# Optimization experiments

Measured on AMD Instinct MI355X. Metric: run time of the kernel, lower is better.

The kernel has to match this reference:

```python
import jax, jax.numpy as jnp
import numpy as np

EPS = 1e-5  # torch GroupNorm default


def setup_inputs() -> dict:
    key = jax.random.key(0)
    ks = jax.random.split(key, 6)
    C = 256
    B, F, H, W = 1, 8, 32, 32
    scale = 1.0 / np.sqrt(C)  # keep logits well-scaled
    return {
        "x": jax.random.normal(ks[0], (B, C, F, H, W), dtype=jnp.float32),
        "gn_w": jnp.ones((C,), jnp.float32),
        "gn_b": jnp.zeros((C,), jnp.float32),
        "qw": jax.random.normal(ks[1], (C, C), jnp.float32) * scale,
        "qb": jnp.zeros((C,), jnp.float32),
        "kw": jax.random.normal(ks[2], (C, C), jnp.float32) * scale,
        "kb": jnp.zeros((C,), jnp.float32),
        "vw": jax.random.normal(ks[3], (C, C), jnp.float32) * scale,
        "vb": jnp.zeros((C,), jnp.float32),
        "ow": jax.random.normal(ks[4], (C, C), jnp.float32) * scale,
        "ob": jnp.zeros((C,), jnp.float32),
    }


def reference(x, gn_w, gn_b, qw, qb, kw, kb, vw, vb, ow, ob):
    B, C, F, H, W = x.shape
    N = F * H * W
    # GroupNorm(1, C): normalize over (C,F,H,W) per sample, per-channel affine
    mean = jnp.mean(x, axis=(1, 2, 3, 4), keepdims=True)
    var = jnp.var(x, axis=(1, 2, 3, 4), keepdims=True)
    xn = (x - mean) * jax.lax.rsqrt(var + EPS)
    xn = xn * gn_w[None, :, None, None, None] + gn_b[None, :, None, None, None]
    xf = xn.reshape(B, C, N)  # [B, C, N]
    # 1x1x1 Conv3d == channel matmul
    q = jnp.einsum('oc,bcn->bon', qw, xf) + qb[None, :, None]
    k = jnp.einsum('oc,bcn->bon', kw, xf) + kb[None, :, None]
    v = jnp.einsum('oc,bcn->bon', vw, xf) + vb[None, :, None]
    # scores[b, n_q, n_k] = q^T k, scaled by C^-0.5
    scores = jnp.einsum('bcn,bcm->bnm', q, k) * (C ** -0.5)
    weights = jax.nn.softmax(scores, axis=-1)  # over keys
    # attention[b, c, n_q] = sum_m v[b,c,m] * weights[b,n_q,m]
    att = jnp.einsum('bcm,bnm->bcn', v, weights)
    att = jnp.einsum('oc,bcn->bon', ow, att) + ob[None, :, None]
    return xn + att.reshape(B, C, F, H, W)
```

## Files before the change

### kernel.cpp

```cpp
#include <hip/hip_runtime.h>
#include <hip/hip_bf16.h>
#include <cstdint>

#define NSP 8192
#define CCH 256
#define KBLK 32
#define NSPLIT 8
#define KEYS_PER_SPLIT 1024
#define NTILES 32

typedef __attribute__((ext_vector_type(4))) float f32x4;
typedef __attribute__((ext_vector_type(16))) float f32x16;
typedef __attribute__((ext_vector_type(8))) short bf16x8;
typedef __attribute__((ext_vector_type(2))) unsigned int u32x2;

__device__ __forceinline__ ushort f2bf(float f) {
  union { float f; uint32_t u; } v; v.f = f;
  uint32_t r = (v.u + 0x7FFFu + ((v.u >> 16) & 1u)) >> 16;
  return (ushort)r;
}
__device__ __forceinline__ float bf2f(ushort u) {
  union { uint32_t u; float f; } v; v.u = ((uint32_t)u) << 16; return v.f;
}
__device__ __forceinline__ uint32_t pk2bf(float lo, float hi) {
  __hip_bfloat162 h = __float22bfloat162_rn({lo, hi});
  union { __hip_bfloat162 h; uint32_t u; } c; c.h = h; return c.u;
}

__device__ __forceinline__ void gload_lds16(const void* g, void* l) {
  auto gp = (const __attribute__((address_space(1))) uint32_t*)(uintptr_t)g;
  auto lp = (__attribute__((address_space(3))) uint32_t*)(uint32_t)(uintptr_t)l;
  __builtin_amdgcn_global_load_lds(gp, lp, 16, 0, 0);
}

__device__ __forceinline__ void perm32swap(uint32_t& a, uint32_t& b) {
#if __has_builtin(__builtin_amdgcn_permlane32_swap)
  u32x2 r = __builtin_amdgcn_permlane32_swap(a, b, false, false);
  a = r[0]; b = r[1];
#else
  uint32_t sa = __shfl_xor((int)a, 32), sb = __shfl_xor((int)b, 32);
  bool lo = (threadIdx.x & 63) < 32;
  uint32_t na = lo ? a : sb;
  uint32_t nb = lo ? sa : b;
  a = na; b = nb;
#endif
}

__global__ __launch_bounds__(256) void k_stats1(const float* __restrict__ x,
                                                float* __restrict__ part) {
  int t = threadIdx.x, b = blockIdx.x;
  float s = 0.f, ss = 0.f;
  const float4* x4 = (const float4*)x;
  for (int i = 0; i < 4; ++i) {
    float4 v = x4[(size_t)i * 131072 + b * 256 + t];
    s += v.x + v.y + v.z + v.w;
    ss += v.x * v.x + v.y * v.y + v.z * v.z + v.w * v.w;
  }
  for (int m = 1; m < 64; m <<= 1) { s += __shfl_xor(s, m); ss += __shfl_xor(ss, m); }
  __shared__ float ls[4], lss[4];
  int w = t >> 6, lane = t & 63;
  if (lane == 0) { ls[w] = s; lss[w] = ss; }
  __syncthreads();
  if (t == 0) {
    part[b * 2 + 0] = ls[0] + ls[1] + ls[2] + ls[3];
    part[b * 2 + 1] = lss[0] + lss[1] + lss[2] + lss[3];
  }
}

__global__ __launch_bounds__(256) void k_castw(const float* __restrict__ qw, const float* __restrict__ kw,
                                               const float* __restrict__ vw, const float* __restrict__ ow,
                                               ushort* __restrict__ wqkv, ushort* __restrict__ wo,
                                               const float* __restrict__ part, float* __restrict__ stat) {
  if (blockIdx.x == 1024) {
    int t = threadIdx.x;
    float s = 0.f, ss = 0.f;
    for (int i = t; i < 512; i += 256) { s += part[i * 2]; ss += part[i * 2 + 1]; }
    for (int m = 1; m < 64; m <<= 1) { s += __shfl_xor(s, m); ss += __shfl_xor(ss, m); }
    __shared__ float ls[4], lss[4];
    int w = t >> 6, lane = t & 63;
    if (lane == 0) { ls[w] = s; lss[w] = ss; }
    __syncthreads();
    if (t == 0) {
      float sum = ls[0] + ls[1] + ls[2] + ls[3];
      float ssum = lss[0] + lss[1] + lss[2] + lss[3];
      float mean = sum * (1.f / 2097152.f);
      float var = ssum * (1.f / 2097152.f) - mean * mean;
      stat[0] = mean;
      stat[1] = rsqrtf(var + 1e-5f);
    }
    return;
  }
  int idx = blockIdx.x * 256 + threadIdx.x;
  if (idx < 65536) wqkv[idx] = f2bf(qw[idx]);
  else if (idx < 131072) wqkv[idx] = f2bf(kw[idx - 65536]);
  else if (idx < 196608) wqkv[idx] = f2bf(vw[idx - 131072]);
  else wo[idx - 196608] = f2bf(ow[idx - 196608]);
}

__global__ __launch_bounds__(256) void k_norm_t(const float* __restrict__ x,
                                                const float* __restrict__ gw, const float* __restrict__ gb,
                                                const float* __restrict__ stat, ushort* __restrict__ xnT) {
  __shared__ float tile[64][66];
  int n0 = blockIdx.x * 64, c0 = blockIdx.y * 64;
  int t = threadIdx.x, colr = t & 63, rq = t >> 6;
  float mean = stat[0], rinv = stat[1];
  for (int rr = 0; rr < 16; ++rr) {
    int row = rr * 4 + rq;
    int c = c0 + row;
    float v = x[(size_t)c * NSP + n0 + colr];
    tile[row][colr] = (v - mean) * rinv * gw[c] + gb[c];
  }
  __syncthreads();
  for (int rr = 0; rr < 16; ++rr) {
    int rowW = rr * 4 + rq;
    xnT[(size_t)(n0 + rowW) * 256 + c0 + colr] = f2bf(tile[colr][rowW]);
  }
}

__global__ __launch_bounds__(256) void k_qkv(const ushort* __restrict__ xnT, const ushort* __restrict__ wqkv,
                                             const float* __restrict__ qb, const float* __restrict__ kb,
                                             const float* __restrict__ vb,
                                             ushort* __restrict__ qT, ushort* __restrict__ k_tiles,
                                             ushort* __restrict__ v_tiles) {
  __shared__ ushort tile[64][80];
  int nb = blockIdx.x, ob = blockIdx.y;
  int w = threadIdx.x >> 6, lane = threadIdx.x & 63;
  int l16 = lane & 15, kgrp = lane >> 4;
  int n_row = nb * 64 + w * 16 + l16;
  bf16x8 a[8];
  const bf16x8* arow = (const bf16x8*)(xnT + (size_t)n_row * 256);
  for (int ks = 0; ks < 8; ++ks) a[ks] = arow[ks * 4 + kgrp];
  f32x4 acc[4];
  for (int ct = 0; ct < 4; ++ct) {
    int o = ob * 64 + ct * 16 + l16;
    const bf16x8* brow = (const bf16x8*)(wqkv + (size_t)o * 256);
    f32x4 c = {0.f, 0.f, 0.f, 0.f};
    for (int ks = 0; ks < 8; ++ks)
      c = __builtin_amdgcn_mfma_f32_16x16x32_bf16(a[ks], brow[ks * 4 + kgrp], c, 0, 0, 0);
    acc[ct] = c;
  }
  const float SCALE = 0.0625f * 1.44269504088896340736f;
  if (ob < 4) {
    for (int ct = 0; ct < 4; ++ct) {
      int o = ob * 64 + ct * 16 + l16;
      for (int r = 0; r < 4; ++r) {
        int n = nb * 64 + w * 16 + kgrp * 4 + r;
        qT[(size_t)n * 256 + o] = f2bf((acc[ct][r] + qb[o]) * SCALE);
      }
    }
  } else if (ob < 8) {
    for (int ct = 0; ct < 4; ++ct) {
      int o_l = ct * 16 + l16;
      for (int r = 0; r < 4; ++r) {
        int n_l = w * 16 + kgrp * 4 + r;
        tile[n_l][o_l] = f2bf(acc[ct][r] + kb[(ob - 4) * 64 + o_l]);
      }
    }
    __syncthreads();
    for (int j = 0; j < 2; ++j) {
      int idx = j * 256 + threadIdx.x;
      int tile_l = idx >> 8, s = (idx >> 5) & 7, key = idx & 31;
      size_t off = (size_t)(nb * 2 + tile_l) * 16384 +
                   (size_t)((ob - 4) * 8 + s) * 512 + key * 16;
      *(uint4*)((char*)k_tiles + off) = *(const uint4*)&tile[tile_l * 32 + key][s * 8];
    }
  } else {
    for (int ct = 0; ct < 4; ++ct) {
      int o_l = ct * 16 + l16;
      for (int r = 0; r < 4; ++r) {
        int n_l = w * 16 + kgrp * 4 + r;
        tile[o_l][n_l] = f2bf(acc[ct][r] + vb[(ob - 8) * 64 + o_l]);
      }
    }
    __syncthreads();
    for (int j = 0; j < 2; ++j) {
      int idx = j * 256 + threadIdx.x;
      int tile_l = idx >> 8, slot = (idx >> 6) & 3, c_l = idx & 63;
      size_t off = (size_t)(nb * 2 + tile_l) * 8192 + slot * 2048 +
                   (size_t)((ob - 8) * 64 + c_l) * 8;
      *(uint4*)((char*)v_tiles + off * 2) = *(const uint4*)&tile[c_l][tile_l * 32 + slot * 8];
    }
  }
}

__global__ __launch_bounds__(512, 2) void k_attn(const ushort* __restrict__ qT, const ushort* __restrict__ k_tiles,
                                                 const ushort* __restrict__ v_tiles,
                                                 ushort* __restrict__ Opart, float* __restrict__ mpart,
                                                 float* __restrict__ lpart) {
  __shared__ __align__(16) ushort SMEM[32768];
  ushort* k_lds = SMEM;
  ushort* v_lds = SMEM + 16384;

  int bid = blockIdx.x;
  int split = bid & 7, qblk = bid >> 3;
  int t = threadIdx.x, w = t >> 6, lane = t & 63;
  int l31 = lane & 31, lhi = lane >> 5;
  int q0w = qblk * 256 + w * 32;

  bf16x8 qf[16];
  {
    const char* qbase = (const char*)qT + (size_t)(q0w + l31) * 512;
#pragma unroll
    for (int cs = 0; cs < 16; ++cs)
      qf[cs] = *(const bf16x8*)(qbase + cs * 32 + lhi * 16);
  }

  f32x16 acc[8] = {};
  float m_r = -1e30f, l_p = 0.f;
  bf16x8 pf0, pf1;

  const char* kT_b = (const char*)k_tiles + (size_t)split * KEYS_PER_SPLIT * 512;
  const char* v_b = (const char*)v_tiles + (size_t)split * KEYS_PER_SPLIT * 512;

  auto STAGE_K = [&](int tt) {
    const char* ksrc = kT_b + (size_t)tt * 16384 + w * 2048;
    char* kdst = (char*)(k_lds + (tt & 1) * 8192) + w * 2048;
#pragma unroll
    for (int i = 0; i < 2; ++i)
      gload_lds16(ksrc + i * 1024 + lane * 16, kdst + i * 1024);
  };
  auto STAGE_V = [&](int tt) {
    char* vdst = (char*)(v_lds + (tt & 1) * 8192) + w * 2048;
    const char* vsrc = v_b + (size_t)tt * 16384 + w * 2048;
#pragma unroll
    for (int i = 0; i < 2; ++i)
      gload_lds16(vsrc + i * 1024 + lane * 16, vdst + i * 1024);
  };

  auto SOFTMAX_PACK = [&](f32x16& S0) {
    float x0 = fmaxf(S0[0], S0[1]), x1 = fmaxf(S0[2], S0[3]);
    float x2 = fmaxf(S0[4], S0[5]), x3 = fmaxf(S0[6], S0[7]);
    float x4 = fmaxf(S0[8], S0[9]), x5 = fmaxf(S0[10], S0[11]);
    float x6 = fmaxf(S0[12], S0[13]), x7 = fmaxf(S0[14], S0[15]);
    float pm = fmaxf(fmaxf(fmaxf(x0, x1), fmaxf(x2, x3)),
                     fmaxf(fmaxf(x4, x5), fmaxf(x6, x7)));
    pm = fmaxf(pm, __shfl_xor(pm, 32));
    if (!__all(pm <= m_r + 8.f)) {
      float mn = fmaxf(m_r, pm);
      float alpha = __builtin_amdgcn_exp2f(m_r - mn);
      m_r = mn;
      l_p *= alpha;
#pragma unroll
      for (int cb = 0; cb < 8; ++cb)
#pragma unroll
        for (int r = 0; r < 16; ++r) acc[cb][r] *= alpha;
    }
    {
      float t0s = 0.f, t1s = 0.f, t2s = 0.f, t3s = 0.f;
#pragma unroll
      for (int r = 0; r < 16; ++r) {
        S0[r] = __builtin_amdgcn_exp2f(S0[r] - m_r);
        if (r < 4) t0s += S0[r];
        else if (r < 8) t1s += S0[r];
        else if (r < 12) t2s += S0[r];
        else t3s += S0[r];
      }
      l_p += (t0s + t1s) + (t2s + t3s);
    }
    union { uint32_t w[4]; bf16x8 v; } u;
    {
      uint32_t x = pk2bf(S0[0], S0[1]), y = pk2bf(S0[4], S0[5]);
      perm32swap(x, y);
      uint32_t x2_ = pk2bf(S0[2], S0[3]), y2 = pk2bf(S0[6], S0[7]);
      perm32swap(x2_, y2);
      u.w[0] = x; u.w[1] = x2_; u.w[2] = y; u.w[3] = y2;
      pf0 = u.v;
    }
    {
      uint32_t x = pk2bf(S0[8], S0[9]), y = pk2bf(S0[12], S0[13]);
      perm32swap(x, y);
      uint32_t x2_ = pk2bf(S0[10], S0[11]), y2 = pk2bf(S0[14], S0[15]);
      perm32swap(x2_, y2);
      u.w[0] = x; u.w[1] = x2_; u.w[2] = y; u.w[3] = y2;
      pf1 = u.v;
    }
  };

  STAGE_K(0);

  asm volatile("s_waitcnt vmcnt(0) lgkmcnt(0)" ::: "memory");
  __builtin_amdgcn_s_barrier();
  __builtin_amdgcn_sched_barrier(0);
  STAGE_K(1);
  STAGE_V(0);
  {
    const ushort* kl = k_lds;
    f32x16 S0 = {};
    __builtin_amdgcn_s_setprio(1);
#pragma unroll
    for (int cs = 0; cs < 16; ++cs) {
      int slot = cs * 2 + lhi;
      bf16x8 a0 = *(const bf16x8*)(kl + slot * 256 + l31 * 8);
      S0 = __builtin_amdgcn_mfma_f32_32x32x16_bf16(a0, qf[cs], S0, 0, 0, 0);
    }
    __builtin_amdgcn_s_setprio(0);
    SOFTMAX_PACK(S0);
  }

#pragma unroll 1
  for (int tt = 1; tt < NTILES; ++tt) {
    asm volatile("s_waitcnt vmcnt(0) lgkmcnt(0)" ::: "memory");
    __builtin_amdgcn_s_barrier();
    __builtin_amdgcn_sched_barrier(0);
    if (tt + 1 < NTILES) STAGE_K(tt + 1);
    STAGE_V(tt);

    const ushort* kl = k_lds + (tt & 1) * 8192;
    const ushort* vl = v_lds + ((tt - 1) & 1) * 8192;
    f32x16 S0 = {};
    __builtin_amdgcn_s_setprio(1);
#pragma unroll
    for (int cb = 0; cb < 8; ++cb) {
      bf16x8 va0 = *(const bf16x8*)(vl + (0 + lhi) * 2048 + (cb * 32 + l31) * 8);
      acc[cb] = __builtin_amdgcn_mfma_f32_32x32x16_bf16(va0, pf0, acc[cb], 0, 0, 0);
      {
        int slot = 4 * cb + lhi;
        bf16x8 ka = *(const bf16x8*)(kl + slot * 256 + l31 * 8);
        S0 = __builtin_amdgcn_mfma_f32_32x32x16_bf16(ka, qf[2 * cb], S0, 0, 0, 0);
      }
      bf16x8 va1 = *(const bf16x8*)(vl + (2 + lhi) * 2048 + (cb * 32 + l31) * 8);
      acc[cb] = __builtin_amdgcn_mfma_f32_32x32x16_bf16(va1, pf1, acc[cb], 0, 0, 0);
      {
        int slot = 4 * cb + 2 + lhi;
        bf16x8 ka = *(const bf16x8*)(kl + slot * 256 + l31 * 8);
        S0 = __builtin_amdgcn_mfma_f32_32x32x16_bf16(ka, qf[2 * cb + 1], S0, 0, 0, 0);
      }
    }
    __builtin_amdgcn_s_setprio(0);
    SOFTMAX_PACK(S0);
  }

  asm volatile("s_waitcnt vmcnt(0) lgkmcnt(0)" ::: "memory");
  __builtin_amdgcn_s_barrier();
  {
    const ushort* vl = v_lds + ((NTILES - 1) & 1) * 8192;
    __builtin_amdgcn_s_setprio(1);
#pragma unroll
    for (int cb = 0; cb < 8; ++cb) {
      bf16x8 va0 = *(const bf16x8*)(vl + (0 + lhi) * 2048 + (cb * 32 + l31) * 8);
      acc[cb] = __builtin_amdgcn_mfma_f32_32x32x16_bf16(va0, pf0, acc[cb], 0, 0, 0);
      bf16x8 va1 = *(const bf16x8*)(vl + (2 + lhi) * 2048 + (cb * 32 + l31) * 8);
      acc[cb] = __builtin_amdgcn_mfma_f32_32x32x16_bf16(va1, pf1, acc[cb], 0, 0, 0);
    }
    __builtin_amdgcn_s_setprio(0);
  }

  asm volatile("s_waitcnt lgkmcnt(0)" ::: "memory");
  __builtin_amdgcn_s_barrier();

  float l_tot = l_p + __shfl_xor(l_p, 32);

  char* eb = (char*)SMEM + w * 4608;
  size_t gq0 = (size_t)split * NSP + q0w;
#pragma unroll
  for (int ch = 0; ch < 4; ++ch) {
#pragma unroll
    for (int cb2 = 0; cb2 < 2; ++cb2) {
      int cb = ch * 2 + cb2;
#pragma unroll
      for (int g = 0; g < 4; ++g) {
        int cl = cb2 * 32 + g * 8 + 4 * lhi;
        *(uint32_t*)(eb + l31 * 144 + cl * 2) = pk2bf(acc[cb][g * 4 + 0], acc[cb][g * 4 + 1]);
        *(uint32_t*)(eb + l31 * 144 + cl * 2 + 4) = pk2bf(acc[cb][g * 4 + 2], acc[cb][g * 4 + 3]);
      }
    }
    asm volatile("s_waitcnt lgkmcnt(0)" ::: "memory");
    __builtin_amdgcn_sched_barrier(0);
#pragma unroll
    for (int i = 0; i < 4; ++i) {
      int flat = i * 1024 + lane * 16;
      int qr = flat >> 7, off = flat & 127;
      uint4 val = *(const uint4*)(eb + qr * 144 + off);
      *(uint4*)((char*)Opart + (gq0 + qr) * 512 + ch * 128 + off) = val;
    }
    asm volatile("s_waitcnt lgkmcnt(0)" ::: "memory");
    __builtin_amdgcn_sched_barrier(0);
  }
  if (lane < 32) {
    int q = q0w + l31;
    mpart[split * NSP + q] = m_r;
    lpart[split * NSP + q] = l_tot;
  }
}

__global__ __launch_bounds__(256) void k_combine(const ushort* __restrict__ Opart,
                                                 const float* __restrict__ mpart,
                                                 const float* __restrict__ lpart,
                                                 ushort* __restrict__ attT) {
  int q = blockIdx.x * 8 + (threadIdx.x >> 5);
  int c8 = threadIdx.x & 31;
  float M = -1e30f;
#pragma unroll
  for (int s = 0; s < NSPLIT; ++s) M = fmaxf(M, mpart[s * NSP + q]);
  float L = 0.f;
  float av[8] = {};
#pragma unroll
  for (int s = 0; s < NSPLIT; ++s) {
    float ws = __builtin_amdgcn_exp2f(mpart[s * NSP + q] - M);
    L += ws * lpart[s * NSP + q];
    bf16x8 o = *(const bf16x8*)(Opart + ((size_t)s * NSP + q) * 256 + c8 * 8);
#pragma unroll
    for (int j = 0; j < 8; ++j) av[j] += ws * bf2f((ushort)o[j]);
  }
  float rL = 1.f / L;
  uint4 outv;
  outv.x = pk2bf(av[0] * rL, av[1] * rL);
  outv.y = pk2bf(av[2] * rL, av[3] * rL);
  outv.z = pk2bf(av[4] * rL, av[5] * rL);
  outv.w = pk2bf(av[6] * rL, av[7] * rL);
  *(uint4*)(attT + (size_t)q * 256 + c8 * 8) = outv;
}

__global__ __launch_bounds__(256) void k_final(const ushort* __restrict__ attT, const ushort* __restrict__ wo,
                                               const float* __restrict__ ob, const float* __restrict__ x,
                                               const float* __restrict__ gw, const float* __restrict__ gb,
                                               const float* __restrict__ stat, float* __restrict__ out) {
  int nb = blockIdx.x, obk = blockIdx.y;
  int w = threadIdx.x >> 6, lane = threadIdx.x & 63;
  int l16 = lane & 15, kgrp = lane >> 4;
  int orow = obk * 64 + w * 16 + l16;
  bf16x8 a[8];
  const bf16x8* arow = (const bf16x8*)(wo + (size_t)orow * 256);
  for (int ks = 0; ks < 8; ++ks) a[ks] = arow[ks * 4 + kgrp];
  float mean = stat[0], rinv = stat[1];
  f32x4 acc[4];
  for (int ct = 0; ct < 4; ++ct) {
    int n = nb * 64 + ct * 16 + l16;
    const bf16x8* brow = (const bf16x8*)(attT + (size_t)n * 256);
    f32x4 c = {0.f, 0.f, 0.f, 0.f};
    for (int ks = 0; ks < 8; ++ks)
      c = __builtin_amdgcn_mfma_f32_16x16x32_bf16(a[ks], brow[ks * 4 + kgrp], c, 0, 0, 0);
    acc[ct] = c;
  }
  for (int ct = 0; ct < 4; ++ct) {
    for (int r = 0; r < 4; ++r) {
      int o = obk * 64 + w * 16 + kgrp * 4 + r;
      int n = nb * 64 + ct * 16 + l16;
      float xv = x[(size_t)o * NSP + n];
      float xn = (xv - mean) * rinv * gw[o] + gb[o];
      out[(size_t)o * NSP + n] = xn + acc[ct][r] + ob[o];
    }
  }
}

extern "C" void kernel_launch(void* const* d_in, const int* in_sizes, int n_in,
                              void* d_out, int out_size, void* d_ws, size_t ws_size,
                              hipStream_t stream) {
  const float* x = (const float*)d_in[0];
  const float* gw = (const float*)d_in[1];
  const float* gb = (const float*)d_in[2];
  const float* qw = (const float*)d_in[3];
  const float* qbv = (const float*)d_in[4];
  const float* kw = (const float*)d_in[5];
  const float* kbv = (const float*)d_in[6];
  const float* vw = (const float*)d_in[7];
  const float* vbv = (const float*)d_in[8];
  const float* ow = (const float*)d_in[9];
  const float* obv = (const float*)d_in[10];
  float* out = (float*)d_out;
  char* ws = (char*)d_ws;
  const size_t KB = 1024, MB = 1048576;
  float* part = (float*)(ws);
  float* stat = (float*)(ws + 60 * KB);
  ushort* wqkv = (ushort*)(ws + 64 * KB);
  ushort* wo = (ushort*)(ws + 448 * KB);
  float* mpart = (float*)(ws + 64 * KB);
  float* lpart = (float*)(ws + 576 * KB);
  ushort* xnT = (ushort*)(ws + 1 * MB);
  ushort* qT = (ushort*)(ws + 5 * MB);
  ushort* k_tiles = (ushort*)(ws + 9 * MB);
  ushort* v_tiles = (ushort*)(ws + 13 * MB);
  ushort* Opart = (ushort*)(ws + 17 * MB);
  ushort* attT = xnT;

  k_stats1<<<512, 256, 0, stream>>>(x, part);
  k_castw<<<1025, 256, 0, stream>>>(qw, kw, vw, ow, wqkv, wo, part, stat);
  k_norm_t<<<dim3(128, 4), 256, 0, stream>>>(x, gw, gb, stat, xnT);
  k_qkv<<<dim3(128, 12), 256, 0, stream>>>(xnT, wqkv, qbv, kbv, vbv, qT, k_tiles, v_tiles);
  k_attn<<<256, 512, 0, stream>>>(qT, k_tiles, v_tiles, Opart, mpart, lpart);
  k_combine<<<NSP / 8, 256, 0, stream>>>(Opart, mpart, lpart, attT);
  k_final<<<dim3(128, 4), 256, 0, stream>>>(attT, wo, obv, x, gw, gb, stat, out);
}
```

Before: 133.8 us.

## Fuse split combine into output projection and overlap softmax with PV MFMAs

The separate combine kernel, which wrote a bf16 attention buffer, is merged into the final output-projection kernel. It now reduces the split partials into LDS and runs 32x32 MFMAs from there, removing one launch and a global round trip. Inside the attention loop, the QK MFMAs are issued first and the exp2 and max work is interleaved with the second half of the PV MFMAs. The exponentials are computed against the stale running max, and rescaling is deferred until after the tile. The first-tile max now starts from 0 instead of -inf, and correctness relies on the lazy-rescale threshold.

```diff
diff --git a/kernel.cpp b/kernel.cpp
--- a/kernel.cpp
+++ b/kernel.cpp
@@ -206,7 +206,7 @@
   }
 
   f32x16 acc[8] = {};
-  float m_r = -1e30f, l_p = 0.f;
+  float m_r = 0.f, l_p = 0.f;
   bf16x8 pf0, pf1;
 
   const char* kT_b = (const char*)k_tiles + (size_t)split * KEYS_PER_SPLIT * 512;
@@ -227,36 +227,7 @@
       gload_lds16(vsrc + i * 1024 + lane * 16, vdst + i * 1024);
   };
 
-  auto SOFTMAX_PACK = [&](f32x16& S0) {
-    float x0 = fmaxf(S0[0], S0[1]), x1 = fmaxf(S0[2], S0[3]);
-    float x2 = fmaxf(S0[4], S0[5]), x3 = fmaxf(S0[6], S0[7]);
-    float x4 = fmaxf(S0[8], S0[9]), x5 = fmaxf(S0[10], S0[11]);
-    float x6 = fmaxf(S0[12], S0[13]), x7 = fmaxf(S0[14], S0[15]);
-    float pm = fmaxf(fmaxf(fmaxf(x0, x1), fmaxf(x2, x3)),
-                     fmaxf(fmaxf(x4, x5), fmaxf(x6, x7)));
-    pm = fmaxf(pm, __shfl_xor(pm, 32));
-    if (!__all(pm <= m_r + 8.f)) {
-      float mn = fmaxf(m_r, pm);
-      float alpha = __builtin_amdgcn_exp2f(m_r - mn);
-      m_r = mn;
-      l_p *= alpha;
-#pragma unroll
-      for (int cb = 0; cb < 8; ++cb)
-#pragma unroll
-        for (int r = 0; r < 16; ++r) acc[cb][r] *= alpha;
-    }
-    {
-      float t0s = 0.f, t1s = 0.f, t2s = 0.f, t3s = 0.f;
-#pragma unroll
-      for (int r = 0; r < 16; ++r) {
-        S0[r] = __builtin_amdgcn_exp2f(S0[r] - m_r);
-        if (r < 4) t0s += S0[r];
-        else if (r < 8) t1s += S0[r];
-        else if (r < 12) t2s += S0[r];
-        else t3s += S0[r];
-      }
-      l_p += (t0s + t1s) + (t2s + t3s);
-    }
+  auto PACK = [&](const f32x16& S0) {
     union { uint32_t w[4]; bf16x8 v; } u;
     {
       uint32_t x = pk2bf(S0[0], S0[1]), y = pk2bf(S0[4], S0[5]);
@@ -294,7 +265,22 @@
       S0 = __builtin_amdgcn_mfma_f32_32x32x16_bf16(a0, qf[cs], S0, 0, 0, 0);
     }
     __builtin_amdgcn_s_setprio(0);
-    SOFTMAX_PACK(S0);
+    float x0 = fmaxf(S0[0], S0[1]), x1 = fmaxf(S0[2], S0[3]);
+    float x2 = fmaxf(S0[4], S0[5]), x3 = fmaxf(S0[6], S0[7]);
+    float x4 = fmaxf(S0[8], S0[9]), x5 = fmaxf(S0[10], S0[11]);
+    float x6 = fmaxf(S0[12], S0[13]), x7 = fmaxf(S0[14], S0[15]);
+    float pm = fmaxf(fmaxf(fmaxf(x0, x1), fmaxf(x2, x3)),
+                     fmaxf(fmaxf(x4, x5), fmaxf(x6, x7)));
+    pm = fmaxf(pm, __shfl_xor(pm, 32));
+    if (!__all(pm <= m_r + 8.f)) m_r = fmaxf(m_r, pm);
+    float t0s = 0.f, t1s = 0.f;
+#pragma unroll
+    for (int r = 0; r < 16; ++r) {
+      S0[r] = __builtin_amdgcn_exp2f(S0[r] - m_r);
+      if (r & 1) t1s += S0[r]; else t0s += S0[r];
+    }
+    l_p = t0s + t1s;
+    PACK(S0);
   }
 
 #pragma unroll 1
@@ -311,23 +297,47 @@
     __builtin_amdgcn_s_setprio(1);
 #pragma unroll
     for (int cb = 0; cb < 8; ++cb) {
-      bf16x8 va0 = *(const bf16x8*)(vl + (0 + lhi) * 2048 + (cb * 32 + l31) * 8);
+      bf16x8 va0 = *(const bf16x8*)(vl + lhi * 2048 + (cb * 32 + l31) * 8);
       acc[cb] = __builtin_amdgcn_mfma_f32_32x32x16_bf16(va0, pf0, acc[cb], 0, 0, 0);
       {
-        int slot = 4 * cb + lhi;
-        bf16x8 ka = *(const bf16x8*)(kl + slot * 256 + l31 * 8);
+        bf16x8 ka = *(const bf16x8*)(kl + (4 * cb + lhi) * 256 + l31 * 8);
         S0 = __builtin_amdgcn_mfma_f32_32x32x16_bf16(ka, qf[2 * cb], S0, 0, 0, 0);
       }
+      {
+        bf16x8 ka = *(const bf16x8*)(kl + (4 * cb + 2 + lhi) * 256 + l31 * 8);
+        S0 = __builtin_amdgcn_mfma_f32_32x32x16_bf16(ka, qf[2 * cb + 1], S0, 0, 0, 0);
+      }
+    }
+    float pm0 = -1e30f, pm1 = -1e30f;
+    float t0s = 0.f, t1s = 0.f;
+#pragma unroll
+    for (int cb = 0; cb < 8; ++cb) {
       bf16x8 va1 = *(const bf16x8*)(vl + (2 + lhi) * 2048 + (cb * 32 + l31) * 8);
       acc[cb] = __builtin_amdgcn_mfma_f32_32x32x16_bf16(va1, pf1, acc[cb], 0, 0, 0);
-      {
-        int slot = 4 * cb + 2 + lhi;
-        bf16x8 ka = *(const bf16x8*)(kl + slot * 256 + l31 * 8);
-        S0 = __builtin_amdgcn_mfma_f32_32x32x16_bf16(ka, qf[2 * cb + 1], S0, 0, 0, 0);
-      }
+      pm0 = fmaxf(pm0, S0[2 * cb]);
+      S0[2 * cb] = __builtin_amdgcn_exp2f(S0[2 * cb] - m_r);
+      t0s += S0[2 * cb];
+      pm1 = fmaxf(pm1, S0[2 * cb + 1]);
+      S0[2 * cb + 1] = __builtin_amdgcn_exp2f(S0[2 * cb + 1] - m_r);
+      t1s += S0[2 * cb + 1];
     }
     __builtin_amdgcn_s_setprio(0);
-    SOFTMAX_PACK(S0);
+    float pm = fmaxf(pm0, pm1);
+    pm = fmaxf(pm, __shfl_xor(pm, 32));
+    if (!__all(pm <= m_r + 8.f)) {
+      float mn = fmaxf(m_r, pm);
+      float alpha = __builtin_amdgcn_exp2f(m_r - mn);
+      m_r = mn;
+      l_p *= alpha; t0s *= alpha; t1s *= alpha;
+#pragma unroll
+      for (int r = 0; r < 16; ++r) S0[r] *= alpha;
+#pragma unroll
+      for (int cb = 0; cb < 8; ++cb)
+#pragma unroll
+        for (int r = 0; r < 16; ++r) acc[cb][r] *= alpha;
+    }
+    l_p += t0s + t1s;
+    PACK(S0);
   }
 
   asm volatile("s_waitcnt vmcnt(0) lgkmcnt(0)" ::: "memory");
@@ -337,7 +347,7 @@
     __builtin_amdgcn_s_setprio(1);
 #pragma unroll
     for (int cb = 0; cb < 8; ++cb) {
-      bf16x8 va0 = *(const bf16x8*)(vl + (0 + lhi) * 2048 + (cb * 32 + l31) * 8);
+      bf16x8 va0 = *(const bf16x8*)(vl + lhi * 2048 + (cb * 32 + l31) * 8);
       acc[cb] = __builtin_amdgcn_mfma_f32_32x32x16_bf16(va0, pf0, acc[cb], 0, 0, 0);
       bf16x8 va1 = *(const bf16x8*)(vl + (2 + lhi) * 2048 + (cb * 32 + l31) * 8);
       acc[cb] = __builtin_amdgcn_mfma_f32_32x32x16_bf16(va1, pf1, acc[cb], 0, 0, 0);
@@ -383,62 +393,73 @@
   }
 }
 
-__global__ __launch_bounds__(256) void k_combine(const ushort* __restrict__ Opart,
-                                                 const float* __restrict__ mpart,
-                                                 const float* __restrict__ lpart,
-                                                 ushort* __restrict__ attT) {
-  int q = blockIdx.x * 8 + (threadIdx.x >> 5);
-  int c8 = threadIdx.x & 31;
-  float M = -1e30f;
-#pragma unroll
-  for (int s = 0; s < NSPLIT; ++s) M = fmaxf(M, mpart[s * NSP + q]);
-  float L = 0.f;
-  float av[8] = {};
-#pragma unroll
-  for (int s = 0; s < NSPLIT; ++s) {
-    float ws = __builtin_amdgcn_exp2f(mpart[s * NSP + q] - M);
-    L += ws * lpart[s * NSP + q];
-    bf16x8 o = *(const bf16x8*)(Opart + ((size_t)s * NSP + q) * 256 + c8 * 8);
-#pragma unroll
-    for (int j = 0; j < 8; ++j) av[j] += ws * bf2f((ushort)o[j]);
-  }
-  float rL = 1.f / L;
-  uint4 outv;
-  outv.x = pk2bf(av[0] * rL, av[1] * rL);
-  outv.y = pk2bf(av[2] * rL, av[3] * rL);
-  outv.z = pk2bf(av[4] * rL, av[5] * rL);
-  outv.w = pk2bf(av[6] * rL, av[7] * rL);
-  *(uint4*)(attT + (size_t)q * 256 + c8 * 8) = outv;
-}
-
-__global__ __launch_bounds__(256) void k_final(const ushort* __restrict__ attT, const ushort* __restrict__ wo,
-                                               const float* __restrict__ ob, const float* __restrict__ x,
-                                               const float* __restrict__ gw, const float* __restrict__ gb,
-                                               const float* __restrict__ stat, float* __restrict__ out) {
-  int nb = blockIdx.x, obk = blockIdx.y;
-  int w = threadIdx.x >> 6, lane = threadIdx.x & 63;
-  int l16 = lane & 15, kgrp = lane >> 4;
-  int orow = obk * 64 + w * 16 + l16;
-  bf16x8 a[8];
-  const bf16x8* arow = (const bf16x8*)(wo + (size_t)orow * 256);
-  for (int ks = 0; ks < 8; ++ks) a[ks] = arow[ks * 4 + kgrp];
+__global__ __launch_bounds__(512) void k_finalc(const ushort* __restrict__ Opart,
+                                                const float* __restrict__ mpart,
+                                                const float* __restrict__ lpart,
+                                                const ushort* __restrict__ wo,
+                                                const float* __restrict__ ob,
+                                                const float* __restrict__ x,
+                                                const float* __restrict__ gw, const float* __restrict__ gb,
+                                                const float* __restrict__ stat,
+                                                float* __restrict__ out) {
+  __shared__ __align__(16) ushort attL[32][64][8];
+  __shared__ float wtab[8][64];
+  int nb = blockIdx.x;
+  int t = threadIdx.x, w = t >> 6, lane = t & 63;
+  int l31 = lane & 31, lhi = lane >> 5;
   float mean = stat[0], rinv = stat[1];
-  f32x4 acc[4];
-  for (int ct = 0; ct < 4; ++ct) {
-    int n = nb * 64 + ct * 16 + l16;
-    const bf16x8* brow = (const bf16x8*)(attT + (size_t)n * 256);
-    f32x4 c = {0.f, 0.f, 0.f, 0.f};
-    for (int ks = 0; ks < 8; ++ks)
-      c = __builtin_amdgcn_mfma_f32_16x16x32_bf16(a[ks], brow[ks * 4 + kgrp], c, 0, 0, 0);
-    acc[ct] = c;
-  }
-  for (int ct = 0; ct < 4; ++ct) {
-    for (int r = 0; r < 4; ++r) {
-      int o = obk * 64 + w * 16 + kgrp * 4 + r;
-      int n = nb * 64 + ct * 16 + l16;
+
+  if (t < 64) {
+    int n = nb * 64 + t;
+    float mv[8], M = -1e30f;
+#pragma unroll
+    for (int s = 0; s < 8; ++s) { mv[s] = mpart[s * NSP + n]; M = fmaxf(M, mv[s]); }
+    float L = 0.f, wv[8];
+#pragma unroll
+    for (int s = 0; s < 8; ++s) {
+      wv[s] = __builtin_amdgcn_exp2f(mv[s] - M);
+      L += wv[s] * lpart[s * NSP + n];
+    }
+    float rL = 1.f / L;
+#pragma unroll
+    for (int s = 0; s < 8; ++s) wtab[s][t] = wv[s] * rL;
+  }
+  __syncthreads();
+#pragma unroll
+  for (int i = 0; i < 4; ++i) {
+    int flat = i * 512 + t;
+    int n = flat >> 5, c8 = flat & 31;
+    float av[8] = {};
+#pragma unroll
+    for (int s = 0; s < 8; ++s) {
+      float wn = wtab[s][n];
+      bf16x8 o8 = *(const bf16x8*)(Opart + ((size_t)s * NSP + nb * 64 + n) * 256 + c8 * 8);
+#pragma unroll
+      for (int j = 0; j < 8; ++j) av[j] += wn * bf2f((ushort)o8[j]);
+    }
+    uint4 pk;
+    pk.x = pk2bf(av[0], av[1]); pk.y = pk2bf(av[2], av[3]);
+    pk.z = pk2bf(av[4], av[5]); pk.w = pk2bf(av[6], av[7]);
+    *(uint4*)&attL[c8][n][0] = pk;
+  }
+  __syncthreads();
+  int obase = w * 32;
+#pragma unroll
+  for (int half = 0; half < 2; ++half) {
+    f32x16 c = {};
+#pragma unroll
+    for (int cs = 0; cs < 16; ++cs) {
+      bf16x8 a = *(const bf16x8*)(wo + (size_t)(obase + l31) * 256 + cs * 16 + lhi * 8);
+      bf16x8 b = *(const bf16x8*)&attL[cs * 2 + lhi][half * 32 + l31][0];
+      c = __builtin_amdgcn_mfma_f32_32x32x16_bf16(a, b, c, 0, 0, 0);
+    }
+#pragma unroll
+    for (int r = 0; r < 16; ++r) {
+      int o = obase + (r & 3) + 8 * (r >> 2) + 4 * lhi;
+      int n = nb * 64 + half * 32 + l31;
       float xv = x[(size_t)o * NSP + n];
       float xn = (xv - mean) * rinv * gw[o] + gb[o];
-      out[(size_t)o * NSP + n] = xn + acc[ct][r] + ob[o];
+      out[(size_t)o * NSP + n] = xn + c[r] + ob[o];
     }
   }
 }
@@ -471,13 +492,11 @@
   ushort* k_tiles = (ushort*)(ws + 9 * MB);
   ushort* v_tiles = (ushort*)(ws + 13 * MB);
   ushort* Opart = (ushort*)(ws + 17 * MB);
-  ushort* attT = xnT;
 
   k_stats1<<<512, 256, 0, stream>>>(x, part);
   k_castw<<<1025, 256, 0, stream>>>(qw, kw, vw, ow, wqkv, wo, part, stat);
   k_norm_t<<<dim3(128, 4), 256, 0, stream>>>(x, gw, gb, stat, xnT);
   k_qkv<<<dim3(128, 12), 256, 0, stream>>>(xnT, wqkv, qbv, kbv, vbv, qT, k_tiles, v_tiles);
   k_attn<<<256, 512, 0, stream>>>(qT, k_tiles, v_tiles, Opart, mpart, lpart);
-  k_combine<<<NSP / 8, 256, 0, stream>>>(Opart, mpart, lpart, attT);
-  k_final<<<dim3(128, 4), 256, 0, stream>>>(attT, wo, obv, x, gw, gb, stat, out);
-}
+  k_finalc<<<128, 512, 0, stream>>>(Opart, mpart, lpart, wo, obv, x, gw, gb, stat, out);
+}
```

Result: slower. 142.7 us (+6.7%).

## Overlap speculative exp2 with second-half PV MFMAs in attention loop

Applied to the files above, without the earlier changes.

Restructures the main loop so all QK MFMAs for a tile are issued first. The max, exp2 and row-sum for the new scores are then interleaved with the second half of the PV MFMAs, using the previous running max speculatively. When the max grows beyond the threshold, the already-exponentiated scores, partial sums and accumulators are rescaled afterwards. The goal is to hide softmax VALU/transcendental latency under matrix work, at the cost of an extra rescale of S0 on the rare correction path. The running max now starts at 0 and the first tile initializes it directly.

```diff
diff --git a/kernel.cpp b/kernel.cpp
--- a/kernel.cpp
+++ b/kernel.cpp
@@ -206,7 +206,7 @@
   }
 
   f32x16 acc[8] = {};
-  float m_r = -1e30f, l_p = 0.f;
+  float m_r = 0.f, l_p = 0.f;
   bf16x8 pf0, pf1;
 
   const char* kT_b = (const char*)k_tiles + (size_t)split * KEYS_PER_SPLIT * 512;
@@ -227,36 +227,7 @@
       gload_lds16(vsrc + i * 1024 + lane * 16, vdst + i * 1024);
   };
 
-  auto SOFTMAX_PACK = [&](f32x16& S0) {
-    float x0 = fmaxf(S0[0], S0[1]), x1 = fmaxf(S0[2], S0[3]);
-    float x2 = fmaxf(S0[4], S0[5]), x3 = fmaxf(S0[6], S0[7]);
-    float x4 = fmaxf(S0[8], S0[9]), x5 = fmaxf(S0[10], S0[11]);
-    float x6 = fmaxf(S0[12], S0[13]), x7 = fmaxf(S0[14], S0[15]);
-    float pm = fmaxf(fmaxf(fmaxf(x0, x1), fmaxf(x2, x3)),
-                     fmaxf(fmaxf(x4, x5), fmaxf(x6, x7)));
-    pm = fmaxf(pm, __shfl_xor(pm, 32));
-    if (!__all(pm <= m_r + 8.f)) {
-      float mn = fmaxf(m_r, pm);
-      float alpha = __builtin_amdgcn_exp2f(m_r - mn);
-      m_r = mn;
-      l_p *= alpha;
-#pragma unroll
-      for (int cb = 0; cb < 8; ++cb)
-#pragma unroll
-        for (int r = 0; r < 16; ++r) acc[cb][r] *= alpha;
-    }
-    {
-      float t0s = 0.f, t1s = 0.f, t2s = 0.f, t3s = 0.f;
-#pragma unroll
-      for (int r = 0; r < 16; ++r) {
-        S0[r] = __builtin_amdgcn_exp2f(S0[r] - m_r);
-        if (r < 4) t0s += S0[r];
-        else if (r < 8) t1s += S0[r];
-        else if (r < 12) t2s += S0[r];
-        else t3s += S0[r];
-      }
-      l_p += (t0s + t1s) + (t2s + t3s);
-    }
+  auto PACK = [&](const f32x16& S0) {
     union { uint32_t w[4]; bf16x8 v; } u;
     {
       uint32_t x = pk2bf(S0[0], S0[1]), y = pk2bf(S0[4], S0[5]);
@@ -294,7 +265,22 @@
       S0 = __builtin_amdgcn_mfma_f32_32x32x16_bf16(a0, qf[cs], S0, 0, 0, 0);
     }
     __builtin_amdgcn_s_setprio(0);
-    SOFTMAX_PACK(S0);
+    float x0 = fmaxf(S0[0], S0[1]), x1 = fmaxf(S0[2], S0[3]);
+    float x2 = fmaxf(S0[4], S0[5]), x3 = fmaxf(S0[6], S0[7]);
+    float x4 = fmaxf(S0[8], S0[9]), x5 = fmaxf(S0[10], S0[11]);
+    float x6 = fmaxf(S0[12], S0[13]), x7 = fmaxf(S0[14], S0[15]);
+    float pm = fmaxf(fmaxf(fmaxf(x0, x1), fmaxf(x2, x3)),
+                     fmaxf(fmaxf(x4, x5), fmaxf(x6, x7)));
+    pm = fmaxf(pm, __shfl_xor(pm, 32));
+    if (!__all(pm <= m_r + 8.f)) m_r = fmaxf(m_r, pm);
+    float t0s = 0.f, t1s = 0.f;
+#pragma unroll
+    for (int r = 0; r < 16; ++r) {
+      S0[r] = __builtin_amdgcn_exp2f(S0[r] - m_r);
+      if (r & 1) t1s += S0[r]; else t0s += S0[r];
+    }
+    l_p = t0s + t1s;
+    PACK(S0);
   }
 
 #pragma unroll 1
@@ -311,23 +297,47 @@
     __builtin_amdgcn_s_setprio(1);
 #pragma unroll
     for (int cb = 0; cb < 8; ++cb) {
-      bf16x8 va0 = *(const bf16x8*)(vl + (0 + lhi) * 2048 + (cb * 32 + l31) * 8);
+      bf16x8 va0 = *(const bf16x8*)(vl + lhi * 2048 + (cb * 32 + l31) * 8);
       acc[cb] = __builtin_amdgcn_mfma_f32_32x32x16_bf16(va0, pf0, acc[cb], 0, 0, 0);
       {
-        int slot = 4 * cb + lhi;
-        bf16x8 ka = *(const bf16x8*)(kl + slot * 256 + l31 * 8);
+        bf16x8 ka = *(const bf16x8*)(kl + (4 * cb + lhi) * 256 + l31 * 8);
         S0 = __builtin_amdgcn_mfma_f32_32x32x16_bf16(ka, qf[2 * cb], S0, 0, 0, 0);
       }
+      {
+        bf16x8 ka = *(const bf16x8*)(kl + (4 * cb + 2 + lhi) * 256 + l31 * 8);
+        S0 = __builtin_amdgcn_mfma_f32_32x32x16_bf16(ka, qf[2 * cb + 1], S0, 0, 0, 0);
+      }
+    }
+    float pm0 = -1e30f, pm1 = -1e30f;
+    float t0s = 0.f, t1s = 0.f;
+#pragma unroll
+    for (int cb = 0; cb < 8; ++cb) {
       bf16x8 va1 = *(const bf16x8*)(vl + (2 + lhi) * 2048 + (cb * 32 + l31) * 8);
       acc[cb] = __builtin_amdgcn_mfma_f32_32x32x16_bf16(va1, pf1, acc[cb], 0, 0, 0);
-      {
-        int slot = 4 * cb + 2 + lhi;
-        bf16x8 ka = *(const bf16x8*)(kl + slot * 256 + l31 * 8);
-        S0 = __builtin_amdgcn_mfma_f32_32x32x16_bf16(ka, qf[2 * cb + 1], S0, 0, 0, 0);
-      }
+      pm0 = fmaxf(pm0, S0[2 * cb]);
+      S0[2 * cb] = __builtin_amdgcn_exp2f(S0[2 * cb] - m_r);
+      t0s += S0[2 * cb];
+      pm1 = fmaxf(pm1, S0[2 * cb + 1]);
+      S0[2 * cb + 1] = __builtin_amdgcn_exp2f(S0[2 * cb + 1] - m_r);
+      t1s += S0[2 * cb + 1];
     }
     __builtin_amdgcn_s_setprio(0);
-    SOFTMAX_PACK(S0);
+    float pm = fmaxf(pm0, pm1);
+    pm = fmaxf(pm, __shfl_xor(pm, 32));
+    if (!__all(pm <= m_r + 8.f)) {
+      float mn = fmaxf(m_r, pm);
+      float alpha = __builtin_amdgcn_exp2f(m_r - mn);
+      m_r = mn;
+      l_p *= alpha; t0s *= alpha; t1s *= alpha;
+#pragma unroll
+      for (int r = 0; r < 16; ++r) S0[r] *= alpha;
+#pragma unroll
+      for (int cb = 0; cb < 8; ++cb)
+#pragma unroll
+        for (int r = 0; r < 16; ++r) acc[cb][r] *= alpha;
+    }
+    l_p += t0s + t1s;
+    PACK(S0);
   }
 
   asm volatile("s_waitcnt vmcnt(0) lgkmcnt(0)" ::: "memory");
@@ -337,7 +347,7 @@
     __builtin_amdgcn_s_setprio(1);
 #pragma unroll
     for (int cb = 0; cb < 8; ++cb) {
-      bf16x8 va0 = *(const bf16x8*)(vl + (0 + lhi) * 2048 + (cb * 32 + l31) * 8);
+      bf16x8 va0 = *(const bf16x8*)(vl + lhi * 2048 + (cb * 32 + l31) * 8);
       acc[cb] = __builtin_amdgcn_mfma_f32_32x32x16_bf16(va0, pf0, acc[cb], 0, 0, 0);
       bf16x8 va1 = *(const bf16x8*)(vl + (2 + lhi) * 2048 + (cb * 32 + l31) * 8);
       acc[cb] = __builtin_amdgcn_mfma_f32_32x32x16_bf16(va1, pf1, acc[cb], 0, 0, 0);
```

New measurement: 131.9 us. About the same (-1.4%).
